# Optimization experiments

Measured on AMD Instinct MI355X. Metric: run time of the kernel, lower is better.

The kernel has to match this reference:

```python
import jax, jax.numpy as jnp
import numpy as np

D_MODEL = 768
N_HEAD = 12
BATCH = 2
SEQ = 2048
MASK_FILL = -100000.0


def setup_inputs() -> dict:
    key = jax.random.key(0)
    ks = jax.random.split(key, 10)
    s = 1.0 / np.sqrt(D_MODEL)
    inp = {
        "xEnc": jax.random.normal(ks[0], (BATCH, SEQ, D_MODEL), jnp.float32),
        "xDec": jax.random.normal(ks[1], (BATCH, SEQ, D_MODEL), jnp.float32),
        # causal mask: True where attention is disallowed (j > i)
        "mask": (jnp.arange(SEQ)[None, :] > jnp.arange(SEQ)[:, None])[None, None, :, :],
        "wQ": jax.random.uniform(ks[2], (D_MODEL, D_MODEL), jnp.float32, -s, s),
        "bQ": jax.random.uniform(ks[3], (D_MODEL,), jnp.float32, -s, s),
        "wK": jax.random.uniform(ks[4], (D_MODEL, D_MODEL), jnp.float32, -s, s),
        "bK": jax.random.uniform(ks[5], (D_MODEL,), jnp.float32, -s, s),
        "wV": jax.random.uniform(ks[6], (D_MODEL, D_MODEL), jnp.float32, -s, s),
        "bV": jax.random.uniform(ks[7], (D_MODEL,), jnp.float32, -s, s),
        "wOut": jax.random.uniform(ks[8], (D_MODEL, D_MODEL), jnp.float32, -s, s),
        "bOut": jax.random.uniform(ks[9], (D_MODEL,), jnp.float32, -s, s),
    }
    return inp


def reference(xEnc, xDec, mask, wQ, bQ, wK, bK, wV, bV, wOut, bOut):
    B, S, D = xEnc.shape
    H = N_HEAD
    Dh = D // H
    # torch Linear: y = x @ W.T + b
    Q = xDec @ wQ.T + bQ
    K = xEnc @ wK.T + bK
    V = xEnc @ wV.T + bV
    Q = Q.reshape(B, S, H, Dh).transpose(0, 2, 1, 3)  # [B,H,S,Dh]
    K = K.reshape(B, S, H, Dh).transpose(0, 2, 1, 3)
    V = V.reshape(B, S, H, Dh).transpose(0, 2, 1, 3)
    score = jnp.einsum("bhqd,bhkd->bhqk", Q, K) / jnp.sqrt(jnp.float32(Dh))
    score = jnp.where(mask, MASK_FILL, score)
    attn = jax.nn.softmax(score, axis=-1)
    ctx = jnp.einsum("bhqk,bhkd->bhqd", attn, V)  # [B,H,S,Dh]
    ctx = ctx.transpose(0, 2, 1, 3).reshape(B, S, D)
    return ctx @ wOut.T + bOut
```

## Files before the change

### kernel.cpp

```cpp
#include <hip/hip_runtime.h>
#include <stdint.h>
#include <stddef.h>

#define DMODEL 768
#define NHEAD 12
#define SEQLEN 2048
#define NBATCH 2
#define DH 64
#define MTOT (NBATCH*SEQLEN)

typedef short s16x4 __attribute__((ext_vector_type(4)));
typedef short s16x8 __attribute__((ext_vector_type(8)));
typedef float f32x4 __attribute__((ext_vector_type(4)));

#define XDECB_OFF 0u
#define XENCB_OFF 3145728u
#define WQB_OFF   6291456u
#define WKB_OFF   6881280u
#define WVB_OFF   7471104u
#define WOUTB_OFF 8060928u
#define QB_OFF    8650752u
#define KB_OFF    11796480u
#define VT_OFF    14942208u
#define CTXB_OFF  18087936u

#define QSCALE 0.18033688011112042f

static __device__ __forceinline__ unsigned short f2bf(float f) {
  union { float f; unsigned int u; } v; v.f = f;
  unsigned int r = v.u + 0x7fffu + ((v.u >> 16) & 1u);
  return (unsigned short)(r >> 16);
}

static __device__ __forceinline__ unsigned int pack2bf(float f0, float f1) {
  union { float f; unsigned int u; } a, b; a.f = f0; b.f = f1;
  return __builtin_amdgcn_perm(b.u + 0x8000u, a.u + 0x8000u, 0x07060302u);
}

#if __has_builtin(__builtin_amdgcn_exp2f)
#define EXP2(x) __builtin_amdgcn_exp2f(x)
#else
#define EXP2(x) exp2f(x)
#endif

static __device__ __forceinline__ f32x4 mfma16(s16x4 a, s16x4 b, f32x4 c) {
  return __builtin_amdgcn_mfma_f32_16x16x16bf16_1k(a, b, c, 0, 0, 0);
}
static __device__ __forceinline__ f32x4 mfma32(s16x8 a, s16x8 b, f32x4 c) {
  return __builtin_amdgcn_mfma_f32_16x16x32_bf16(a, b, c, 0, 0, 0);
}

typedef __attribute__((address_space(3))) unsigned int lds_u32_t;
typedef const __attribute__((address_space(1))) unsigned int glb_u32_t;
static __device__ __forceinline__ void gl_lds16(const unsigned short* g,
                                                unsigned short* l) {
  __builtin_amdgcn_global_load_lds((glb_u32_t*)g, (lds_u32_t*)l, 16, 0, 0);
}

__global__ __launch_bounds__(256) void cvt_kernel(
    const float* __restrict__ xDec, const float* __restrict__ xEnc,
    const float* __restrict__ wQ, const float* __restrict__ wK,
    const float* __restrict__ wV, const float* __restrict__ wOut,
    unsigned short* __restrict__ ws)
{
  const int seg = blockIdx.y;
  const float* src;
  unsigned int n4, off;
  switch (seg) {
    case 0:  src = xDec; n4 = 786432; off = XDECB_OFF; break;
    case 1:  src = xEnc; n4 = 786432; off = XENCB_OFF; break;
    case 2:  src = wQ;   n4 = 147456; off = WQB_OFF;   break;
    case 3:  src = wK;   n4 = 147456; off = WKB_OFF;   break;
    case 4:  src = wV;   n4 = 147456; off = WVB_OFF;   break;
    default: src = wOut; n4 = 147456; off = WOUTB_OFF; break;
  }
  unsigned short* d = ws + off;
  const unsigned int stride = gridDim.x * blockDim.x;
  for (unsigned int i = blockIdx.x * blockDim.x + threadIdx.x; i < n4; i += stride) {
    const float4 v = ((const float4*)src)[i];
    s16x4 p;
    p[0] = (short)f2bf(v.x); p[1] = (short)f2bf(v.y);
    p[2] = (short)f2bf(v.z); p[3] = (short)f2bf(v.w);
    ((s16x4*)d)[i] = p;
  }
}

#define BK 64
#define NKT (DMODEL / BK)

__global__ __launch_bounds__(256, 3) void qkv_gemm(
    const unsigned short* __restrict__ xDecB, const unsigned short* __restrict__ xEncB,
    const unsigned short* __restrict__ wQB, const unsigned short* __restrict__ wKB,
    const unsigned short* __restrict__ wVB,
    const float* __restrict__ bQ, const float* __restrict__ bK, const float* __restrict__ bV,
    unsigned short* __restrict__ Qb, unsigned short* __restrict__ Kb,
    unsigned short* __restrict__ Vt)
{
  const int z = blockIdx.z;
  const unsigned short* __restrict__ A = (z == 0) ? xDecB : xEncB;
  const unsigned short* __restrict__ B = (z == 0) ? wQB : ((z == 1) ? wKB : wVB);
  const float* __restrict__ bias = (z == 0) ? bQ : ((z == 1) ? bK : bV);

  __shared__ unsigned short lA[3][64 * BK];
  __shared__ unsigned short lB[3][64 * BK];

  const int tid  = threadIdx.x;
  const int lane = tid & 63;
  const int wid  = tid >> 6;
  const int ln   = lane & 15;
  const int qd   = lane >> 4;
  const int m0 = blockIdx.x * 64;
  const int n0 = blockIdx.y * 64;
  const int wm = (wid & 1) * 32;
  const int wn = (wid >> 1) * 32;

  int srow[2], scol[2];
  #pragma unroll
  for (int c = 0; c < 2; ++c) {
    const int s = c * 256 + wid * 64 + lane;
    srow[c] = s >> 3;
    scol[c] = (((s & 7) ^ ((s >> 3) & 7)) * 8);
  }

  auto stage = [&](int buf, int k0) {
    #pragma unroll
    for (int c = 0; c < 2; ++c) {
      const int ldsoff = (c * 256 + wid * 64) * 8;
      gl_lds16(A + (size_t)(m0 + srow[c]) * DMODEL + k0 + scol[c], &lA[buf][ldsoff]);
      gl_lds16(B + (size_t)(n0 + srow[c]) * DMODEL + k0 + scol[c], &lB[buf][ldsoff]);
    }
  };

  f32x4 acc[2][2] = {};

  stage(0, 0);
  stage(1, BK);

  auto step = [&](int t, int bc, int bs) {
    if (t == NKT - 1) asm volatile("s_waitcnt vmcnt(0)" ::: "memory");
    else              asm volatile("s_waitcnt vmcnt(4)" ::: "memory");
    __builtin_amdgcn_s_barrier();
    __builtin_amdgcn_sched_barrier(0);
    if (t + 2 < NKT) stage(bs, (t + 2) * BK);
    #pragma unroll
    for (int kc = 0; kc < 2; ++kc) {
      s16x8 af[2], bfr[2];
      #pragma unroll
      for (int i = 0; i < 2; ++i) {
        const int r = wm + i * 16 + ln;
        af[i] = *(const s16x8*)&lA[bc][r * 64 + (((kc * 4 + qd) ^ (r & 7)) * 8)];
      }
      #pragma unroll
      for (int j = 0; j < 2; ++j) {
        const int r = wn + j * 16 + ln;
        bfr[j] = *(const s16x8*)&lB[bc][r * 64 + (((kc * 4 + qd) ^ (r & 7)) * 8)];
      }
      #pragma unroll
      for (int i = 0; i < 2; ++i)
        #pragma unroll
        for (int j = 0; j < 2; ++j)
          acc[i][j] = mfma32(af[i], bfr[j], acc[i][j]);
    }
  };

  for (int tb = 0; tb < NKT; tb += 3) {
    step(tb + 0, 0, 2);
    step(tb + 1, 1, 0);
    step(tb + 2, 2, 1);
  }

  #pragma unroll
  for (int j = 0; j < 2; ++j) {
    const int n_g = n0 + wn + j * 16 + ln;
    const float bv = bias[n_g];
    const int h    = n_g >> 6;
    const int dcol = n_g & 63;
    #pragma unroll
    for (int i = 0; i < 2; ++i) {
      #pragma unroll
      for (int r = 0; r < 4; ++r) {
        const int m_g  = m0 + wm + i * 16 + qd * 4 + r;
        const int bb   = m_g >> 11;
        const int srow2 = m_g & 2047;
        const float val = acc[i][j][r] + bv;
        if (z == 0)
          Qb[((size_t)((bb * NHEAD + h) * SEQLEN + srow2)) * DH + dcol] = f2bf(val * QSCALE);
        else if (z == 1)
          Kb[((size_t)((bb * NHEAD + h) * SEQLEN + srow2)) * DH + dcol] = f2bf(val);
        else
          Vt[((size_t)((bb * NHEAD + h) * DH + dcol)) * SEQLEN + srow2] = f2bf(val);
      }
    }
  }
}

__global__ __launch_bounds__(256, 3) void out_gemm(
    const unsigned short* __restrict__ ctx, const unsigned short* __restrict__ wOutB,
    const float* __restrict__ bOut, float* __restrict__ out)
{
  __shared__ unsigned short lA[3][64 * BK];
  __shared__ unsigned short lB[3][64 * BK];

  const int tid  = threadIdx.x;
  const int lane = tid & 63;
  const int wid  = tid >> 6;
  const int ln   = lane & 15;
  const int qd   = lane >> 4;
  const int m0 = blockIdx.x * 64;
  const int n0 = blockIdx.y * 64;
  const int wm = (wid & 1) * 32;
  const int wn = (wid >> 1) * 32;

  int srow[2], scol[2];
  #pragma unroll
  for (int c = 0; c < 2; ++c) {
    const int s = c * 256 + wid * 64 + lane;
    srow[c] = s >> 3;
    scol[c] = (((s & 7) ^ ((s >> 3) & 7)) * 8);
  }

  auto stage = [&](int buf, int k0) {
    #pragma unroll
    for (int c = 0; c < 2; ++c) {
      const int ldsoff = (c * 256 + wid * 64) * 8;
      gl_lds16(ctx + (size_t)(m0 + srow[c]) * DMODEL + k0 + scol[c], &lA[buf][ldsoff]);
      gl_lds16(wOutB + (size_t)(n0 + srow[c]) * DMODEL + k0 + scol[c], &lB[buf][ldsoff]);
    }
  };

  f32x4 acc[2][2] = {};

  stage(0, 0);
  stage(1, BK);

  auto step = [&](int t, int bc, int bs) {
    if (t == NKT - 1) asm volatile("s_waitcnt vmcnt(0)" ::: "memory");
    else              asm volatile("s_waitcnt vmcnt(4)" ::: "memory");
    __builtin_amdgcn_s_barrier();
    __builtin_amdgcn_sched_barrier(0);
    if (t + 2 < NKT) stage(bs, (t + 2) * BK);
    #pragma unroll
    for (int kc = 0; kc < 2; ++kc) {
      s16x8 af[2], bfr[2];
      #pragma unroll
      for (int i = 0; i < 2; ++i) {
        const int r = wm + i * 16 + ln;
        af[i] = *(const s16x8*)&lA[bc][r * 64 + (((kc * 4 + qd) ^ (r & 7)) * 8)];
      }
      #pragma unroll
      for (int j = 0; j < 2; ++j) {
        const int r = wn + j * 16 + ln;
        bfr[j] = *(const s16x8*)&lB[bc][r * 64 + (((kc * 4 + qd) ^ (r & 7)) * 8)];
      }
      #pragma unroll
      for (int i = 0; i < 2; ++i)
        #pragma unroll
        for (int j = 0; j < 2; ++j)
          acc[i][j] = mfma32(af[i], bfr[j], acc[i][j]);
    }
  };

  for (int tb = 0; tb < NKT; tb += 3) {
    step(tb + 0, 0, 2);
    step(tb + 1, 1, 0);
    step(tb + 2, 2, 1);
  }

  #pragma unroll
  for (int j = 0; j < 2; ++j) {
    const int n_g = n0 + wn + j * 16 + ln;
    const float bv = bOut[n_g];
    #pragma unroll
    for (int i = 0; i < 2; ++i) {
      #pragma unroll
      for (int r = 0; r < 4; ++r) {
        const int m_g = m0 + wm + i * 16 + qd * 4 + r;
        out[(size_t)m_g * DMODEL + n_g] = acc[i][j][r] + bv;
      }
    }
  }
}

#define KVT 64
#define VOFF 4096
#define RST 68

__global__ __launch_bounds__(256, 3) void attn_kernel(
    const unsigned short* __restrict__ Qb, const unsigned short* __restrict__ Kb,
    const unsigned short* __restrict__ Vt, unsigned short* __restrict__ ctx,
    float* __restrict__ pout0, float* __restrict__ pout1,
    float* __restrict__ lpart)
{
  __shared__ __attribute__((aligned(16))) unsigned short smem[3][8192];

  const int tid  = threadIdx.x;
  const int lane = tid & 63;
  const int wid  = tid >> 6;
  const int ln   = lane & 15;
  const int qd   = lane >> 4;
  const int qw   = wid & 1;
  const int kw   = wid >> 1;

  const int ord  = blockIdx.x;
  const int xcd  = ord & 7;
  const int slot = ord >> 3;
  const int bh   = xcd * 3 + (slot >> 5);
  const int p    = slot & 31;

  const bool isA = p < 16;
  const int i  = isA ? p : (p - 16);
  const int Ti = (i + 2) >> 1;

  const unsigned short* Kbase = Kb + (size_t)bh * SEQLEN * DH;
  const unsigned short* Vbase = Vt + (size_t)bh * DH * SEQLEN;
  const int bb = bh / NHEAD;
  const int h  = bh % NHEAD;

  float* rO = (float*)&smem[0][0];
  float* rL = rO + 64 * RST;

  auto stage = [&](int b, int kv0) {
    #pragma unroll
    for (int c = 0; c < 2; ++c) {
      const int f = tid + c * 256;
      const int row = f >> 3, sl = f & 7;
      gl_lds16(Kbase + (size_t)(kv0 + row) * DH + ((sl ^ (row & 7)) * 8),
               &smem[b][f * 8]);
    }
    #pragma unroll
    for (int c = 0; c < 2; ++c) {
      const int f = tid + c * 256;
      const int row = f >> 3, sl = f & 7;
      gl_lds16(Vbase + (size_t)row * SEQLEN + kv0 + ((sl ^ (row & 7)) * 8),
               &smem[b][VOFF + f * 8]);
    }
  };

  auto run = [&](int q0, int T0, int NT, int mode) {
    const int t0 = T0 * 2, tend = (T0 + NT) * 2;

    s16x8 Qf[2][2];
    #pragma unroll
    for (int qc = 0; qc < 2; ++qc)
      #pragma unroll
      for (int kc = 0; kc < 2; ++kc)
        Qf[qc][kc] = *(const s16x8*)(Qb +
            ((size_t)bh * SEQLEN + q0 + qw * 32 + qc * 16 + ln) * DH + kc * 32 + qd * 8);

    float l_acc[2] = {};
    f32x4 acc[2][4] = {};

    stage(0, t0 * KVT);
    stage(1, (t0 + 1) * KVT);
    int bc = 0;
    for (int t = t0; t < tend; ++t) {
      if (t + 1 < tend) asm volatile("s_waitcnt vmcnt(4)" ::: "memory");
      else              asm volatile("s_waitcnt vmcnt(0)" ::: "memory");
      __builtin_amdgcn_s_barrier();
      __builtin_amdgcn_sched_barrier(0);
      if (t + 2 < tend) stage(bc >= 1 ? bc - 1 : bc + 2, (t + 2) * KVT);

      const unsigned short* lK = &smem[bc][0];
      const unsigned short* lV = &smem[bc][VOFF];
      const int kv0 = t * KVT;
      const bool diag = (kv0 + KVT > q0);

      s16x4 pf[2][2];
      #pragma unroll
      for (int t8 = 0; t8 < 2; ++t8) {
        const int row = kw * 32 + t8 * 16 + ln;
        const s16x8 k0 = *(const s16x8*)&lK[row * 64 + ((qd ^ (ln & 7)) * 8)];
        const s16x8 k1 = *(const s16x8*)&lK[row * 64 + (((4 + qd) ^ (ln & 7)) * 8)];
        f32x4 sq[2] = {};
        sq[0] = mfma32(k0, Qf[0][0], sq[0]);
        sq[0] = mfma32(k1, Qf[0][1], sq[0]);
        sq[1] = mfma32(k0, Qf[1][0], sq[1]);
        sq[1] = mfma32(k1, Qf[1][1], sq[1]);
        #pragma unroll
        for (int qc = 0; qc < 2; ++qc) {
          if (diag) {
            #pragma unroll
            for (int r = 0; r < 4; ++r) {
              const int kv = kv0 + kw * 32 + t8 * 16 + qd * 4 + r;
              const int q  = q0 + qw * 32 + qc * 16 + ln;
              sq[qc][r] = (kv > q) ? -1e30f : sq[qc][r];
            }
          }
          const float p0 = EXP2(sq[qc][0]);
          const float p1 = EXP2(sq[qc][1]);
          const float p2 = EXP2(sq[qc][2]);
          const float p3 = EXP2(sq[qc][3]);
          l_acc[qc] += (p0 + p1) + (p2 + p3);
          union { unsigned int u[2]; s16x4 v; } pk;
          pk.u[0] = pack2bf(p0, p1);
          pk.u[1] = pack2bf(p2, p3);
          pf[t8][qc] = pk.v;
        }
      }

      #pragma unroll
      for (int t8 = 0; t8 < 2; ++t8) {
        #pragma unroll
        for (int dc = 0; dc < 4; ++dc) {
          const int vrow  = dc * 16 + ln;
          const int slotv = (kw * 4 + t8 * 2 + (qd >> 1)) ^ (ln & 7);
          const s16x4 bv = *(const s16x4*)&lV[vrow * 64 + slotv * 8 + (qd & 1) * 4];
          acc[0][dc] = mfma16(pf[t8][0], bv, acc[0][dc]);
          acc[1][dc] = mfma16(pf[t8][1], bv, acc[1][dc]);
        }
      }
      bc = bc < 2 ? bc + 1 : 0;
    }
    __syncthreads();

    #pragma unroll
    for (int qc = 0; qc < 2; ++qc) {
      l_acc[qc] += __shfl_xor(l_acc[qc], 16);
      l_acc[qc] += __shfl_xor(l_acc[qc], 32);
    }

    if (kw == 1) {
      if (lane < 16) {
        rL[qw * 32 + lane]      = l_acc[0];
        rL[qw * 32 + 16 + lane] = l_acc[1];
      }
      #pragma unroll
      for (int qc = 0; qc < 2; ++qc)
        #pragma unroll
        for (int dc = 0; dc < 4; ++dc)
          #pragma unroll
          for (int r = 0; r < 4; ++r)
            rO[(qw * 32 + qc * 16 + qd * 4 + r) * RST + dc * 16 + ln] =
                acc[qc][dc][r];
    }
    __syncthreads();
    if (kw == 0) {
      #pragma unroll
      for (int qc = 0; qc < 2; ++qc) {
        l_acc[qc] += rL[qw * 32 + qc * 16 + ln];
        #pragma unroll
        for (int dc = 0; dc < 4; ++dc)
          #pragma unroll
          for (int r = 0; r < 4; ++r)
            acc[qc][dc][r] +=
                rO[(qw * 32 + qc * 16 + qd * 4 + r) * RST + dc * 16 + ln];
      }
      if (mode == 0) {
        #pragma unroll
        for (int qc = 0; qc < 2; ++qc) {
          #pragma unroll
          for (int r = 0; r < 4; ++r) {
            const float lr  = __shfl(l_acc[qc], qd * 4 + r);
            const float inv = 1.0f / lr;
            const int q_g = q0 + qw * 32 + qc * 16 + qd * 4 + r;
            unsigned short* dst =
                ctx + ((size_t)bb * SEQLEN + q_g) * DMODEL + h * DH;
            #pragma unroll
            for (int dc = 0; dc < 4; ++dc)
              dst[dc * 16 + ln] = f2bf(acc[qc][dc][r] * inv);
          }
        }
      } else {
        float* PO = (mode == 1) ? pout1 : pout0;
        float* LO = lpart + ((mode == 1) ? (24 * 1024) : 0);
        const int qbase = q0 - 1024 + qw * 32;
        if (lane < 16) {
          LO[bh * 1024 + qbase + lane]      = l_acc[0];
          LO[bh * 1024 + qbase + 16 + lane] = l_acc[1];
        }
        #pragma unroll
        for (int qc = 0; qc < 2; ++qc)
          #pragma unroll
          for (int dc = 0; dc < 4; ++dc)
            #pragma unroll
            for (int r = 0; r < 4; ++r)
              PO[((size_t)bh * 1024 + qbase + qc * 16 + qd * 4 + r) * 64 +
                 dc * 16 + ln] = acc[qc][dc][r];
      }
    }
    __syncthreads();
  };

  if (isA) {
    run(i * 64, 0, Ti, 0);
    run((31 - i) * 64, 0, 9 - Ti, 1);
  } else {
    run((31 - i) * 64, 9 - Ti, 8, 2);
  }
}

__global__ __launch_bounds__(256) void norm_kernel(
    const float* __restrict__ pout0, const float* __restrict__ pout1,
    const float* __restrict__ lpart, unsigned short* __restrict__ ctx)
{
  const int e4  = blockIdx.x * 256 + threadIdx.x;
  const int d4  = e4 & 15;
  const int row = e4 >> 4;
  const int bh  = row >> 10;
  const int qr  = row & 1023;
  const float l = lpart[row] + lpart[24 * 1024 + row];
  const float inv = 1.0f / l;
  const float4 a = ((const float4*)pout0)[e4];
  const float4 b = ((const float4*)pout1)[e4];
  const int bb = bh / NHEAD;
  const int h  = bh % NHEAD;
  unsigned short* dst =
      ctx + ((size_t)bb * SEQLEN + 1024 + qr) * DMODEL + h * DH + d4 * 4;
  s16x4 o;
  o[0] = (short)f2bf((a.x + b.x) * inv);
  o[1] = (short)f2bf((a.y + b.y) * inv);
  o[2] = (short)f2bf((a.z + b.z) * inv);
  o[3] = (short)f2bf((a.w + b.w) * inv);
  *(s16x4*)dst = o;
}

extern "C" void kernel_launch(void* const* d_in, const int* in_sizes, int n_in,
                              void* d_out, int out_size, void* d_ws, size_t ws_size,
                              hipStream_t stream)
{
  const float* xEnc = (const float*)d_in[0];
  const float* xDec = (const float*)d_in[1];
  const float* wQ   = (const float*)d_in[3];
  const float* bQ   = (const float*)d_in[4];
  const float* wK   = (const float*)d_in[5];
  const float* bK   = (const float*)d_in[6];
  const float* wV   = (const float*)d_in[7];
  const float* bV   = (const float*)d_in[8];
  const float* wOut = (const float*)d_in[9];
  const float* bOut = (const float*)d_in[10];

  unsigned short* ws = (unsigned short*)d_ws;
  float* pout0 = (float*)(ws + XDECB_OFF);
  float* pout1 = (float*)(ws + XENCB_OFF);
  float* lpart = (float*)(ws + WQB_OFF);

  cvt_kernel<<<dim3(512, 6), 256, 0, stream>>>(xDec, xEnc, wQ, wK, wV, wOut, ws);
  qkv_gemm<<<dim3(MTOT / 64, DMODEL / 64, 3), 256, 0, stream>>>(
      ws + XDECB_OFF, ws + XENCB_OFF, ws + WQB_OFF, ws + WKB_OFF, ws + WVB_OFF,
      bQ, bK, bV, ws + QB_OFF, ws + KB_OFF, ws + VT_OFF);
  attn_kernel<<<dim3(768), 256, 0, stream>>>(
      ws + QB_OFF, ws + KB_OFF, ws + VT_OFF, ws + CTXB_OFF,
      pout0, pout1, lpart);
  norm_kernel<<<dim3((24 * 1024 * 16) / 256), 256, 0, stream>>>(
      pout0, pout1, lpart, ws + CTXB_OFF);
  out_gemm<<<dim3(MTOT / 64, DMODEL / 64), 256, 0, stream>>>(
      ws + CTXB_OFF, ws + WOUTB_OFF, bOut, (float*)d_out);
}
```

Measured before the change: 176.2 us.

## Fuse split-KV normalization into output GEMM A-tile staging

Removes the separate norm kernel that combined the two partial attention outputs and wrote bf16 ctx for the upper half of the sequence. The out_gemm blocks covering those rows now read the fp32 partials and l sums directly, normalize and convert them to bf16, and write the result into LDS as the A tile. Those blocks use a simpler double-buffered loop with register-staged loads in place of the async triple-buffer. This saves one launch and the ctx write/read round trip. The cost is that each n-column block re-reads the fp32 partials, which doubles A traffic 12-fold across the grid, and global-load latency is exposed in the staging path.

```diff
diff --git a/kernel.cpp b/kernel.cpp
--- a/kernel.cpp
+++ b/kernel.cpp
@@ -196,7 +196,9 @@
 
 __global__ __launch_bounds__(256, 3) void out_gemm(
     const unsigned short* __restrict__ ctx, const unsigned short* __restrict__ wOutB,
-    const float* __restrict__ bOut, float* __restrict__ out)
+    const float* __restrict__ bOut, float* __restrict__ out,
+    const float* __restrict__ pout0, const float* __restrict__ pout1,
+    const float* __restrict__ lpart)
 {
   __shared__ unsigned short lA[3][64 * BK];
   __shared__ unsigned short lB[3][64 * BK];
@@ -210,6 +212,7 @@
   const int n0 = blockIdx.y * 64;
   const int wm = (wid & 1) * 32;
   const int wn = (wid >> 1) * 32;
+  const bool up = (m0 & 1024) != 0;
 
   int srow[2], scol[2];
   #pragma unroll
@@ -219,26 +222,24 @@
     scol[c] = (((s & 7) ^ ((s >> 3) & 7)) * 8);
   }
 
-  auto stage = [&](int buf, int k0) {
+  auto stageB = [&](int buf, int k0) {
+    #pragma unroll
+    for (int c = 0; c < 2; ++c) {
+      const int ldsoff = (c * 256 + wid * 64) * 8;
+      gl_lds16(wOutB + (size_t)(n0 + srow[c]) * DMODEL + k0 + scol[c], &lB[buf][ldsoff]);
+    }
+  };
+  auto stageA = [&](int buf, int k0) {
     #pragma unroll
     for (int c = 0; c < 2; ++c) {
       const int ldsoff = (c * 256 + wid * 64) * 8;
       gl_lds16(ctx + (size_t)(m0 + srow[c]) * DMODEL + k0 + scol[c], &lA[buf][ldsoff]);
-      gl_lds16(wOutB + (size_t)(n0 + srow[c]) * DMODEL + k0 + scol[c], &lB[buf][ldsoff]);
     }
   };
 
   f32x4 acc[2][2] = {};
 
-  stage(0, 0);
-  stage(1, BK);
-
-  auto step = [&](int t, int bc, int bs) {
-    if (t == NKT - 1) asm volatile("s_waitcnt vmcnt(0)" ::: "memory");
-    else              asm volatile("s_waitcnt vmcnt(4)" ::: "memory");
-    __builtin_amdgcn_s_barrier();
-    __builtin_amdgcn_sched_barrier(0);
-    if (t + 2 < NKT) stage(bs, (t + 2) * BK);
+  auto compute = [&](int bc) {
     #pragma unroll
     for (int kc = 0; kc < 2; ++kc) {
       s16x8 af[2], bfr[2];
@@ -260,10 +261,64 @@
     }
   };
 
-  for (int tb = 0; tb < NKT; tb += 3) {
-    step(tb + 0, 0, 2);
-    step(tb + 1, 1, 0);
-    step(tb + 2, 2, 1);
+  if (!up) {
+    stageA(0, 0); stageB(0, 0);
+    stageA(1, BK); stageB(1, BK);
+    auto step = [&](int t, int bc, int bs) {
+      if (t == NKT - 1) asm volatile("s_waitcnt vmcnt(0)" ::: "memory");
+      else              asm volatile("s_waitcnt vmcnt(4)" ::: "memory");
+      __builtin_amdgcn_s_barrier();
+      __builtin_amdgcn_sched_barrier(0);
+      if (t + 2 < NKT) { stageA(bs, (t + 2) * BK); stageB(bs, (t + 2) * BK); }
+      compute(bc);
+    };
+    for (int tb = 0; tb < NKT; tb += 3) {
+      step(tb + 0, 0, 2);
+      step(tb + 1, 1, 0);
+      step(tb + 2, 2, 1);
+    }
+    __syncthreads();
+  } else {
+    int rbase[2];
+    #pragma unroll
+    for (int c = 0; c < 2; ++c) {
+      const int r_g = m0 + srow[c];
+      rbase[c] = (r_g >> 11) * (NHEAD * 1024) + ((r_g & 2047) - 1024);
+    }
+    auto stageA_up = [&](int buf, int k0) {
+      const int h = k0 >> 6;
+      #pragma unroll
+      for (int c = 0; c < 2; ++c) {
+        const int s    = c * 256 + wid * 64 + lane;
+        const int rowp = rbase[c] + h * 1024;
+        const int f4   = rowp * 16 + (scol[c] >> 2);
+        const float4 a0 = ((const float4*)pout0)[f4];
+        const float4 a1 = ((const float4*)pout0)[f4 + 1];
+        const float4 c0 = ((const float4*)pout1)[f4];
+        const float4 c1 = ((const float4*)pout1)[f4 + 1];
+        const float inv = 1.0f / (lpart[rowp] + lpart[24 * 1024 + rowp]);
+        union { unsigned short us[8]; s16x8 v; } pk;
+        pk.us[0] = f2bf((a0.x + c0.x) * inv);
+        pk.us[1] = f2bf((a0.y + c0.y) * inv);
+        pk.us[2] = f2bf((a0.z + c0.z) * inv);
+        pk.us[3] = f2bf((a0.w + c0.w) * inv);
+        pk.us[4] = f2bf((a1.x + c1.x) * inv);
+        pk.us[5] = f2bf((a1.y + c1.y) * inv);
+        pk.us[6] = f2bf((a1.z + c1.z) * inv);
+        pk.us[7] = f2bf((a1.w + c1.w) * inv);
+        *(s16x8*)&lA[buf][s * 8] = pk.v;
+      }
+    };
+
+    stageA_up(0, 0); stageB(0, 0);
+    __syncthreads();
+    int cur = 0;
+    for (int t = 0; t < NKT; ++t) {
+      if (t + 1 < NKT) { stageB(cur ^ 1, (t + 1) * BK); stageA_up(cur ^ 1, (t + 1) * BK); }
+      compute(cur);
+      __syncthreads();
+      cur ^= 1;
+    }
   }
 
   #pragma unroll
@@ -489,31 +544,6 @@
   }
 }
 
-__global__ __launch_bounds__(256) void norm_kernel(
-    const float* __restrict__ pout0, const float* __restrict__ pout1,
-    const float* __restrict__ lpart, unsigned short* __restrict__ ctx)
-{
-  const int e4  = blockIdx.x * 256 + threadIdx.x;
-  const int d4  = e4 & 15;
-  const int row = e4 >> 4;
-  const int bh  = row >> 10;
-  const int qr  = row & 1023;
-  const float l = lpart[row] + lpart[24 * 1024 + row];
-  const float inv = 1.0f / l;
-  const float4 a = ((const float4*)pout0)[e4];
-  const float4 b = ((const float4*)pout1)[e4];
-  const int bb = bh / NHEAD;
-  const int h  = bh % NHEAD;
-  unsigned short* dst =
-      ctx + ((size_t)bb * SEQLEN + 1024 + qr) * DMODEL + h * DH + d4 * 4;
-  s16x4 o;
-  o[0] = (short)f2bf((a.x + b.x) * inv);
-  o[1] = (short)f2bf((a.y + b.y) * inv);
-  o[2] = (short)f2bf((a.z + b.z) * inv);
-  o[3] = (short)f2bf((a.w + b.w) * inv);
-  *(s16x4*)dst = o;
-}
-
 extern "C" void kernel_launch(void* const* d_in, const int* in_sizes, int n_in,
                               void* d_out, int out_size, void* d_ws, size_t ws_size,
                               hipStream_t stream)
@@ -541,8 +571,7 @@
   attn_kernel<<<dim3(768), 256, 0, stream>>>(
       ws + QB_OFF, ws + KB_OFF, ws + VT_OFF, ws + CTXB_OFF,
       pout0, pout1, lpart);
-  norm_kernel<<<dim3((24 * 1024 * 16) / 256), 256, 0, stream>>>(
-      pout0, pout1, lpart, ws + CTXB_OFF);
   out_gemm<<<dim3(MTOT / 64, DMODEL / 64), 256, 0, stream>>>(
-      ws + CTXB_OFF, ws + WOUTB_OFF, bOut, (float*)d_out);
-}
+      ws + CTXB_OFF, ws + WOUTB_OFF, bOut, (float*)d_out,
+      pout0, pout1, lpart);
+}
```

New measurement: 184.9 us. 4.9% more time.
